# Performance work log

Measured on AMD Instinct MI355X. Metric: run time of the kernel, lower is better.

The kernel has to match this reference:

```python
import jax, jax.numpy as jnp
import numpy as np

D_MODEL = 1024
D_FF = 2048
N_EXPERTS = 8
Z_LOSS_COEF = 0.001


def setup_inputs() -> dict:
    key = jax.random.key(0)
    kx, kr, k1, k3, k2 = jax.random.split(key, 5)
    s_in = 1.0 / np.sqrt(D_MODEL)
    s_ff = 1.0 / np.sqrt(D_FF)
    return {
        "x": jax.random.normal(kx, (4, 2048, D_MODEL), dtype=jnp.float32),
        # router: nn.Linear(d_model, num_experts, bias=False) -> weight [E, D]
        "Wr": jax.random.normal(kr, (N_EXPERTS, D_MODEL), dtype=jnp.float32) * s_in,
        # stacked expert weights, torch Linear layout [out, in]
        "W1": jax.random.normal(k1, (N_EXPERTS, D_FF, D_MODEL), dtype=jnp.float32) * s_in,
        "W3": jax.random.normal(k3, (N_EXPERTS, D_FF, D_MODEL), dtype=jnp.float32) * s_in,
        "W2": jax.random.normal(k2, (N_EXPERTS, D_MODEL, D_FF), dtype=jnp.float32) * s_ff,
    }


def reference(x, Wr, W1, W3, W2):
    B, S, D = x.shape
    E = Wr.shape[0]
    xf = x.reshape(B * S, D)          # [T, D]
    T = xf.shape[0]

    # --- router ---
    logits = xf @ Wr.T                # [T, E]
    probs = jax.nn.softmax(logits, axis=-1)
    top2_p, top2_i = jax.lax.top_k(probs, 2)          # [T, 2]
    top2_p = top2_p / (jnp.sum(top2_p, axis=-1, keepdims=True) + 1e-9)

    # dense gate matrix: zero for unselected experts (same math as index_add combine)
    gates = jnp.zeros((T, E), jnp.float32).at[jnp.arange(T)[:, None], top2_i].add(top2_p)

    # --- experts (SwiGLU), computed per-expert over all tokens, masked by gates ---
    h1 = jax.nn.silu(jnp.einsum('td,efd->etf', xf, W1))   # [E, T, F]
    h3 = jnp.einsum('td,efd->etf', xf, W3)                 # [E, T, F]
    y = jnp.einsum('etf,edf->etd', h1 * h3, W2)            # [E, T, D]
    out = jnp.einsum('etd,te->td', y.astype(jnp.float32), gates)
    out = out.astype(x.dtype).reshape(B, S, D)

    # --- losses ---
    z = jax.nn.logsumexp(logits.astype(jnp.float32), axis=-1)
    router_loss = Z_LOSS_COEF * jnp.mean(z * z)

    importance = jnp.sum(probs.astype(jnp.float32), axis=0) / T   # [E]
    top1 = top2_i[:, 0]
    load = jnp.zeros((E,), jnp.float32).at[top1].add(1.0) / T
    aux_loss = jnp.sum(importance * load) * E

    return out, router_loss, aux_loss
```

## Files before the change

### kernel.cpp

```cpp
#include <hip/hip_runtime.h>
#include <stdint.h>

#define NT 8192
#define DM 1024
#define DF 2048
#define RT_BLOCKS 256

typedef __attribute__((ext_vector_type(8))) short short8;
typedef __attribute__((ext_vector_type(4))) float f32x4;
typedef unsigned short us;

__device__ __forceinline__ us f2bf(float f) {
  uint32_t x = __float_as_uint(f);
  return (us)((x + 0x7fffu + ((x >> 16) & 1u)) >> 16);
}

__device__ __forceinline__ void gload16(const void* g, void* l) {
  __builtin_amdgcn_global_load_lds(
      (const __attribute__((address_space(1))) uint32_t*)g,
      (__attribute__((address_space(3))) uint32_t*)l, 16, 0, 0);
}

__global__ void k_cvtw(const float4* __restrict__ w1, const float4* __restrict__ w3,
                       const float4* __restrict__ w2,
                       ushort4* __restrict__ w13, ushort4* __restrict__ w2bf) {
  int s = blockIdx.y;
  const float4* src = (s == 0) ? w1 : (s == 1) ? w3 : w2;
  int n4 = 8 * DF * DM / 4;
  int i = blockIdx.x * blockDim.x + threadIdx.x;
  int st = gridDim.x * blockDim.x;
  for (; i < n4; i += st) {
    float4 v = src[i];
    ushort4 o;
    o.x = f2bf(v.x); o.y = f2bf(v.y); o.z = f2bf(v.z); o.w = f2bf(v.w);
    if (s == 2) {
      w2bf[i] = o;
    } else {
      int e = i >> 19;
      int rem = i & ((1 << 19) - 1);
      int f = rem >> 8;
      int k4 = rem & 255;
      w13[((size_t)e << 20) + (size_t)(2 * f + s) * 256 + k4] = o;
    }
  }
}

__global__ void k_router(const float* __restrict__ x, const float* __restrict__ wr,
                         int* cntb, int* cnt1, float* imp, float* z2,
                         int* epack, float2* gts, us* __restrict__ xbf) {
  int lane = threadIdx.x & 63;
  int wid = threadIdx.x >> 6;
  const float4* w4 = (const float4*)wr;

  float imp_acc[8] = {0.f, 0.f, 0.f, 0.f, 0.f, 0.f, 0.f, 0.f};
  float z2_acc = 0.f;
  int cb_acc[8] = {0, 0, 0, 0, 0, 0, 0, 0};
  int c1_acc[8] = {0, 0, 0, 0, 0, 0, 0, 0};

  for (int t = blockIdx.x * 4 + wid; t < NT; t += RT_BLOCKS * 4) {
    const float4* x4 = (const float4*)(x + (size_t)t * DM);
    ushort4* xb4 = (ushort4*)(xbf + (size_t)t * DM);
    float4 xv[4];
    #pragma unroll
    for (int j = 0; j < 4; ++j) {
      xv[j] = x4[lane + 64 * j];
      ushort4 o;
      o.x = f2bf(xv[j].x); o.y = f2bf(xv[j].y); o.z = f2bf(xv[j].z); o.w = f2bf(xv[j].w);
      xb4[lane + 64 * j] = o;
    }
    float p[8];
    #pragma unroll
    for (int e = 0; e < 8; ++e) p[e] = 0.f;
    #pragma unroll
    for (int j = 0; j < 4; ++j) {
      #pragma unroll
      for (int e = 0; e < 8; ++e) {
        float4 wv = w4[e * 256 + lane + 64 * j];
        p[e] += xv[j].x * wv.x + xv[j].y * wv.y + xv[j].z * wv.z + xv[j].w * wv.w;
      }
    }
    #pragma unroll
    for (int off = 32; off > 0; off >>= 1) {
      #pragma unroll
      for (int e = 0; e < 8; ++e) p[e] += __shfl_down(p[e], off);
    }
    if (lane == 0) {
      float m = p[0];
      #pragma unroll
      for (int e = 1; e < 8; ++e) m = fmaxf(m, p[e]);
      float pr[8], s = 0.f;
      #pragma unroll
      for (int e = 0; e < 8; ++e) { pr[e] = expf(p[e] - m); s += pr[e]; }
      float inv = 1.f / s;
      #pragma unroll
      for (int e = 0; e < 8; ++e) pr[e] *= inv;
      float z = m + logf(s);
      int e0 = 0; float b0 = p[0];
      #pragma unroll
      for (int e = 1; e < 8; ++e) { if (p[e] > b0) { b0 = p[e]; e0 = e; } }
      int e1 = -1; float b1 = -1e30f;
      #pragma unroll
      for (int e = 0; e < 8; ++e) { if (e != e0 && p[e] > b1) { b1 = p[e]; e1 = e; } }
      float p0 = 0.f, p1 = 0.f;
      #pragma unroll
      for (int e = 0; e < 8; ++e) {
        p0 = (e == e0) ? pr[e] : p0;
        p1 = (e == e1) ? pr[e] : p1;
      }
      float gs = p0 + p1 + 1e-9f;
      epack[t] = e0 | (e1 << 16);
      gts[t] = make_float2(p0 / gs, p1 / gs);
      z2_acc += z * z;
      #pragma unroll
      for (int e = 0; e < 8; ++e) {
        imp_acc[e] += pr[e];
        cb_acc[e] += (e == e0) + (e == e1);
        c1_acc[e] += (e == e0);
      }
    }
  }

  __shared__ float simp[4][8];
  __shared__ float sz2[4];
  __shared__ int scb[4][8];
  __shared__ int sc1[4][8];
  if (lane == 0) {
    #pragma unroll
    for (int e = 0; e < 8; ++e) { simp[wid][e] = imp_acc[e]; scb[wid][e] = cb_acc[e]; sc1[wid][e] = c1_acc[e]; }
    sz2[wid] = z2_acc;
  }
  __syncthreads();
  int tid = threadIdx.x;
  if (tid < 8) {
    float s = simp[0][tid] + simp[1][tid] + simp[2][tid] + simp[3][tid];
    int b = scb[0][tid] + scb[1][tid] + scb[2][tid] + scb[3][tid];
    int o = sc1[0][tid] + sc1[1][tid] + sc1[2][tid] + sc1[3][tid];
    atomicAdd(&imp[tid], s);
    atomicAdd(&cntb[tid], b);
    atomicAdd(&cnt1[tid], o);
  } else if (tid == 8) {
    atomicAdd(z2, sz2[0] + sz2[1] + sz2[2] + sz2[3]);
  }
}

__global__ void k_finalize(const int* cntb, const int* cnt1, const float* imp,
                           const float* z2, int* offs, float* otail) {
  if (threadIdx.x == 0 && blockIdx.x == 0) {
    int o = 0;
    for (int e = 0; e < 8; ++e) { offs[e] = o; o += cntb[e]; }
    otail[0] = 1e-3f * z2[0] / (float)NT;
    float aux = 0.f;
    for (int e = 0; e < 8; ++e)
      aux += (imp[e] / (float)NT) * ((float)cnt1[e] / (float)NT);
    otail[1] = aux * 8.f;
  }
}

__global__ void k_scatter(const int* __restrict__ epack, const float2* __restrict__ gts,
                          const int* __restrict__ offs,
                          int* __restrict__ btok, int* __restrict__ pos) {
  int e = blockIdx.x;
  int lane = threadIdx.x;
  int base = offs[e];
  int run = 0;
  for (int j0 = 0; j0 < 2 * NT; j0 += 64) {
    int j = j0 + lane;
    int t = j >> 1;
    int ep = epack[t];
    int sel = (j & 1) ? (ep >> 16) : (ep & 0xffff);
    bool f = (sel == e);
    unsigned long long m = __ballot(f);
    int rank = __popcll(m & ((1ull << lane) - 1ull));
    if (f) {
      int slot = base + run + rank;
      btok[slot] = t;
      pos[j] = slot;
    }
    run += __popcll(m);
  }
}


__global__ __launch_bounds__(512) void k_ffn1(
    const us* __restrict__ xb, const us* __restrict__ w13,
    const int* __restrict__ offs, const int* __restrict__ cnts,
    const int* __restrict__ btok, us* __restrict__ hg) {
  int e = blockIdx.z;
  int cnt = cnts[e];
  int m0 = blockIdx.y * 256;
  if (m0 >= cnt) return;
  int n0 = blockIdx.x * 256;
  int off = offs[e];
  __shared__ __align__(16) short As[2][8192];
  __shared__ __align__(16) short Bs[2][8192];
  __shared__ int tok[256];
  int tid = threadIdx.x, lane = tid & 63, wid = tid >> 6;
  if (tid < 256) {
    int r = m0 + tid; if (r > cnt - 1) r = cnt - 1;
    tok[tid] = btok[off + r];
  }
  __syncthreads();

  int posun = (lane & 7) ^ ((lane >> 3) & 7);
  int rbase = wid * 16 + ((lane >> 3) << 1) + (posun >> 2);
  int gcol = (posun & 3) * 8;
  const us* w13e = w13 + ((size_t)e << 22);
  const us* aP0 = xb + (size_t)tok[rbase] * DM + gcol;
  const us* aP1 = xb + (size_t)tok[rbase + 128] * DM + gcol;
  const us* bP0 = w13e + (size_t)(n0 + rbase) * DM + gcol;
  const us* bP1 = w13e + (size_t)(n0 + rbase + 128) * DM + gcol;
  int dst0 = wid * 512, dst1 = 4096 + wid * 512;

  int wm = wid >> 2, wn = wid & 3;
  int fr = lane & 15, glog = lane >> 4;
  int pos = (((fr & 1) << 2) | glog) ^ ((fr >> 1) & 7);
  int aoff = (wm * 64 + (fr >> 1)) * 64 + pos * 8;
  int boff = (wn * 32 + (fr >> 1)) * 64 + pos * 8;
  f32x4 acc[8][4] = {};

  const int NK = DM / 64;
  for (int kt = 0; kt < NK; ++kt) {
    int k0 = kt * 64;
    #pragma unroll
    for (int h = 0; h < 2; ++h) {
      int ko = k0 + h * 32;
      gload16(aP0 + ko, &As[h][dst0]);
      gload16(aP1 + ko, &As[h][dst1]);
      gload16(bP0 + ko, &Bs[h][dst0]);
      gload16(bP1 + ko, &Bs[h][dst1]);
    }
    __syncthreads();
    #pragma unroll
    for (int kk = 0; kk < 2; ++kk) {
      short8 a[8], b[4];
      #pragma unroll
      for (int mi = 0; mi < 8; ++mi)
        a[mi] = *(const short8*)&As[kk][aoff + mi * 512];
      #pragma unroll
      for (int ni = 0; ni < 4; ++ni)
        b[ni] = *(const short8*)&Bs[kk][boff + ni * 512];
      #pragma unroll
      for (int mi = 0; mi < 8; ++mi) {
        #pragma unroll
        for (int ni = 0; ni < 4; ++ni)
          acc[mi][ni] = __builtin_amdgcn_mfma_f32_16x16x32_bf16(a[mi], b[ni], acc[mi][ni], 0, 0, 0);
      }
    }
    __syncthreads();
  }

  int c = lane & 15, r4 = (lane >> 4) * 4;
  bool evenc = ((c & 1) == 0);
  #pragma unroll
  for (int mi = 0; mi < 8; ++mi) {
    #pragma unroll
    for (int rg = 0; rg < 4; ++rg) {
      int gr = m0 + wm * 128 + mi * 16 + r4 + rg;
      #pragma unroll
      for (int ni = 0; ni < 4; ++ni) {
        float a1v = acc[mi][ni][rg];
        float a3v = __shfl_xor(a1v, 1);
        if (evenc && gr < cnt) {
          int f = (n0 + wn * 64 + ni * 16 + c) >> 1;
          float h = (a1v / (1.f + __expf(-a1v))) * a3v;
          hg[(size_t)(off + gr) * DF + f] = f2bf(h);
        }
      }
    }
  }
}

__global__ __launch_bounds__(512) void k_ffn2(
    const us* __restrict__ hg, const us* __restrict__ w2b,
    const int* __restrict__ offs, const int* __restrict__ cnts,
    float* __restrict__ ys) {
  int e = blockIdx.z;
  int cnt = cnts[e];
  int m0 = blockIdx.y * 256;
  if (m0 >= cnt) return;
  int n0 = blockIdx.x * 256;
  int off = offs[e];
  __shared__ __align__(16) short As[2][8192];
  __shared__ __align__(16) short Bs[2][8192];
  int tid = threadIdx.x, lane = tid & 63, wid = tid >> 6;

  int posun = (lane & 7) ^ ((lane >> 3) & 7);
  int rbase = wid * 16 + ((lane >> 3) << 1) + (posun >> 2);
  int gcol = (posun & 3) * 8;
  int ar0 = m0 + rbase;       if (ar0 > cnt - 1) ar0 = cnt - 1;
  int ar1 = m0 + rbase + 128; if (ar1 > cnt - 1) ar1 = cnt - 1;
  const us* w2e = w2b + ((size_t)e << 21);
  const us* aP0 = hg + (size_t)(off + ar0) * DF + gcol;
  const us* aP1 = hg + (size_t)(off + ar1) * DF + gcol;
  const us* bP0 = w2e + (size_t)(n0 + rbase) * DF + gcol;
  const us* bP1 = w2e + (size_t)(n0 + rbase + 128) * DF + gcol;
  int dst0 = wid * 512, dst1 = 4096 + wid * 512;

  int wm = wid >> 2, wn = wid & 3;
  int fr = lane & 15, glog = lane >> 4;
  int pos = (((fr & 1) << 2) | glog) ^ ((fr >> 1) & 7);
  int aoff = (wm * 64 + (fr >> 1)) * 64 + pos * 8;
  int boff = (wn * 32 + (fr >> 1)) * 64 + pos * 8;
  f32x4 acc[8][4] = {};

  const int NK = DF / 64;
  for (int kt = 0; kt < NK; ++kt) {
    int k0 = kt * 64;
    #pragma unroll
    for (int h = 0; h < 2; ++h) {
      int ko = k0 + h * 32;
      gload16(aP0 + ko, &As[h][dst0]);
      gload16(aP1 + ko, &As[h][dst1]);
      gload16(bP0 + ko, &Bs[h][dst0]);
      gload16(bP1 + ko, &Bs[h][dst1]);
    }
    __syncthreads();
    #pragma unroll
    for (int kk = 0; kk < 2; ++kk) {
      short8 a[8], b[4];
      #pragma unroll
      for (int mi = 0; mi < 8; ++mi)
        a[mi] = *(const short8*)&As[kk][aoff + mi * 512];
      #pragma unroll
      for (int ni = 0; ni < 4; ++ni)
        b[ni] = *(const short8*)&Bs[kk][boff + ni * 512];
      #pragma unroll
      for (int mi = 0; mi < 8; ++mi) {
        #pragma unroll
        for (int ni = 0; ni < 4; ++ni)
          acc[mi][ni] = __builtin_amdgcn_mfma_f32_16x16x32_bf16(a[mi], b[ni], acc[mi][ni], 0, 0, 0);
      }
    }
    __syncthreads();
  }

  int c = lane & 15, r4 = (lane >> 4) * 4;
  #pragma unroll
  for (int mi = 0; mi < 8; ++mi) {
    #pragma unroll
    for (int rg = 0; rg < 4; ++rg) {
      int gr = m0 + wm * 128 + mi * 16 + r4 + rg;
      if (gr < cnt) {
        float* yrow = ys + (size_t)(off + gr) * DM + n0;
        #pragma unroll
        for (int ni = 0; ni < 4; ++ni)
          yrow[wn * 64 + ni * 16 + c] = acc[mi][ni][rg];
      }
    }
  }
}

__global__ void k_gather(const float* __restrict__ ys, const int* __restrict__ pos,
                         const float2* __restrict__ gts, float* __restrict__ out) {
  int idx = blockIdx.x * blockDim.x + threadIdx.x;
  int t = idx >> 8;
  int d4 = idx & 255;
  float2 g = gts[t];
  const float4* y0 = (const float4*)(ys + (size_t)pos[2 * t] * DM) + d4;
  const float4* y1 = (const float4*)(ys + (size_t)pos[2 * t + 1] * DM) + d4;
  float4 a = *y0, b = *y1, o;
  o.x = g.x * a.x + g.y * b.x;
  o.y = g.x * a.y + g.y * b.y;
  o.z = g.x * a.z + g.y * b.z;
  o.w = g.x * a.w + g.y * b.w;
  ((float4*)out)[idx] = o;
}


extern "C" void kernel_launch(void* const* d_in, const int* in_sizes, int n_in,
                              void* d_out, int out_size, void* d_ws, size_t ws_size,
                              hipStream_t stream) {
  const float* x  = (const float*)d_in[0];
  const float* wr = (const float*)d_in[1];
  const float* w1 = (const float*)d_in[2];
  const float* w3 = (const float*)d_in[3];
  const float* w2 = (const float*)d_in[4];
  float* out = (float*)d_out;

  uint8_t* ws = (uint8_t*)d_ws;
  int*    cntb   = (int*)(ws + 0);
  int*    cnt1   = (int*)(ws + 32);
  int*    offs   = (int*)(ws + 96);
  float*  imp    = (float*)(ws + 128);
  float*  z2     = (float*)(ws + 160);
  int*    epack  = (int*)(ws + 4096);
  float2* gts    = (float2*)(ws + 36864);
  int*    btok   = (int*)(ws + 102400);
  int*    pos    = (int*)(ws + 167936);
  us*     xbf    = (us*)(ws + 233472);
  us*     w13    = (us*)(ws + 17010688);
  us*     w2bf   = (us*)(ws + 84119552);
  us*     hg     = (us*)(ws + 117673984);
  float*  ysb    = (float*)(ws + 17010688);

  hipMemsetAsync(ws, 0, 4096, stream);

  k_cvtw<<<dim3(2048, 3), 256, 0, stream>>>(
      (const float4*)w1, (const float4*)w3, (const float4*)w2,
      (ushort4*)w13, (ushort4*)w2bf);

  k_router<<<RT_BLOCKS, 256, 0, stream>>>(x, wr, cntb, cnt1, imp, z2, epack, gts, xbf);
  k_finalize<<<1, 64, 0, stream>>>(cntb, cnt1, imp, z2, offs, out + (size_t)NT * DM);
  k_scatter<<<8, 64, 0, stream>>>(epack, gts, offs, btok, pos);

  k_ffn1<<<dim3(16, 64, 8), 512, 0, stream>>>(xbf, w13, offs, cntb, btok, hg);
  k_ffn2<<<dim3(4, 64, 8), 512, 0, stream>>>(hg, w2bf, offs, cntb, ysb);
  k_gather<<<NT * DM / 4 / 256, 256, 0, stream>>>(ysb, pos, gts, out);
}
```

Measured before the change: 617.5 us.

## Shrink FFN GEMM tiles to 128x128, store expert outputs as bf16, interleave W1/W3 by 16

```diff
diff --git a/kernel.cpp b/kernel.cpp
--- a/kernel.cpp
+++ b/kernel.cpp
@@ -14,6 +14,9 @@
   uint32_t x = __float_as_uint(f);
   return (us)((x + 0x7fffu + ((x >> 16) & 1u)) >> 16);
 }
+__device__ __forceinline__ float bf2f(us v) {
+  return __uint_as_float(((uint32_t)v) << 16);
+}
 
 __device__ __forceinline__ void gload16(const void* g, void* l) {
   __builtin_amdgcn_global_load_lds(
@@ -23,24 +26,28 @@
 
 __global__ void k_cvtw(const float4* __restrict__ w1, const float4* __restrict__ w3,
                        const float4* __restrict__ w2,
-                       ushort4* __restrict__ w13, ushort4* __restrict__ w2bf) {
+                       short8* __restrict__ w13, short8* __restrict__ w2bf) {
   int s = blockIdx.y;
   const float4* src = (s == 0) ? w1 : (s == 1) ? w3 : w2;
-  int n4 = 8 * DF * DM / 4;
+  int n8 = 8 * DF * DM / 8;
   int i = blockIdx.x * blockDim.x + threadIdx.x;
   int st = gridDim.x * blockDim.x;
-  for (; i < n4; i += st) {
-    float4 v = src[i];
-    ushort4 o;
-    o.x = f2bf(v.x); o.y = f2bf(v.y); o.z = f2bf(v.z); o.w = f2bf(v.w);
+  for (; i < n8; i += st) {
+    float4 va = src[2 * i], vb = src[2 * i + 1];
+    short8 o;
+    o[0] = (short)f2bf(va.x); o[1] = (short)f2bf(va.y);
+    o[2] = (short)f2bf(va.z); o[3] = (short)f2bf(va.w);
+    o[4] = (short)f2bf(vb.x); o[5] = (short)f2bf(vb.y);
+    o[6] = (short)f2bf(vb.z); o[7] = (short)f2bf(vb.w);
     if (s == 2) {
       w2bf[i] = o;
     } else {
-      int e = i >> 19;
-      int rem = i & ((1 << 19) - 1);
-      int f = rem >> 8;
-      int k4 = rem & 255;
-      w13[((size_t)e << 20) + (size_t)(2 * f + s) * 256 + k4] = o;
+      int e = i >> 18;
+      int rem = i & ((1 << 18) - 1);
+      int f = rem >> 7;
+      int k8 = rem & 127;
+      int n = 32 * (f >> 4) + 16 * s + (f & 15);
+      w13[((size_t)e << 19) + (size_t)n * 128 + k8] = o;
     }
   }
 }
@@ -88,13 +95,13 @@
       float m = p[0];
       #pragma unroll
       for (int e = 1; e < 8; ++e) m = fmaxf(m, p[e]);
-      float pr[8], s = 0.f;
-      #pragma unroll
-      for (int e = 0; e < 8; ++e) { pr[e] = expf(p[e] - m); s += pr[e]; }
-      float inv = 1.f / s;
+      float pr[8], sum = 0.f;
+      #pragma unroll
+      for (int e = 0; e < 8; ++e) { pr[e] = expf(p[e] - m); sum += pr[e]; }
+      float inv = 1.f / sum;
       #pragma unroll
       for (int e = 0; e < 8; ++e) pr[e] *= inv;
-      float z = m + logf(s);
+      float z = m + logf(sum);
       int e0 = 0; float b0 = p[0];
       #pragma unroll
       for (int e = 1; e < 8; ++e) { if (p[e] > b0) { b0 = p[e]; e0 = e; } }
@@ -132,10 +139,10 @@
   __syncthreads();
   int tid = threadIdx.x;
   if (tid < 8) {
-    float s = simp[0][tid] + simp[1][tid] + simp[2][tid] + simp[3][tid];
+    float ss = simp[0][tid] + simp[1][tid] + simp[2][tid] + simp[3][tid];
     int b = scb[0][tid] + scb[1][tid] + scb[2][tid] + scb[3][tid];
     int o = sc1[0][tid] + sc1[1][tid] + sc1[2][tid] + sc1[3][tid];
-    atomicAdd(&imp[tid], s);
+    atomicAdd(&imp[tid], ss);
     atomicAdd(&cntb[tid], b);
     atomicAdd(&cnt1[tid], o);
   } else if (tid == 8) {
@@ -181,42 +188,43 @@
 }
 
 
-__global__ __launch_bounds__(512) void k_ffn1(
+__global__ __launch_bounds__(256) void k_ffn1(
     const us* __restrict__ xb, const us* __restrict__ w13,
     const int* __restrict__ offs, const int* __restrict__ cnts,
     const int* __restrict__ btok, us* __restrict__ hg) {
   int e = blockIdx.z;
   int cnt = cnts[e];
-  int m0 = blockIdx.y * 256;
+  int m0 = blockIdx.y * 128;
   if (m0 >= cnt) return;
-  int n0 = blockIdx.x * 256;
+  int n0 = blockIdx.x * 128;
   int off = offs[e];
-  __shared__ __align__(16) short As[2][8192];
-  __shared__ __align__(16) short Bs[2][8192];
-  __shared__ int tok[256];
+  __shared__ __align__(16) short As[2][4096];
+  __shared__ __align__(16) short Bs[2][4096];
+  __shared__ int tok[128];
   int tid = threadIdx.x, lane = tid & 63, wid = tid >> 6;
-  if (tid < 256) {
+  if (tid < 128) {
     int r = m0 + tid; if (r > cnt - 1) r = cnt - 1;
     tok[tid] = btok[off + r];
   }
   __syncthreads();
 
-  int posun = (lane & 7) ^ ((lane >> 3) & 7);
-  int rbase = wid * 16 + ((lane >> 3) << 1) + (posun >> 2);
-  int gcol = (posun & 3) * 8;
+  int prow = tid >> 3;
+  int pu = (tid & 7) ^ (prow & 7);
+  int row0 = prow * 2 + (pu >> 2);
+  int gc = (pu & 3) * 8;
   const us* w13e = w13 + ((size_t)e << 22);
-  const us* aP0 = xb + (size_t)tok[rbase] * DM + gcol;
-  const us* aP1 = xb + (size_t)tok[rbase + 128] * DM + gcol;
-  const us* bP0 = w13e + (size_t)(n0 + rbase) * DM + gcol;
-  const us* bP1 = w13e + (size_t)(n0 + rbase + 128) * DM + gcol;
-  int dst0 = wid * 512, dst1 = 4096 + wid * 512;
-
-  int wm = wid >> 2, wn = wid & 3;
+  const us* a0 = xb + (size_t)tok[row0] * DM + gc;
+  const us* a1 = xb + (size_t)tok[row0 + 64] * DM + gc;
+  const us* b0 = w13e + (size_t)(n0 + row0) * DM + gc;
+  const us* b1 = w13e + (size_t)(n0 + row0 + 64) * DM + gc;
+  int dsl = tid * 8;
+
+  int wm = wid >> 1, wn = wid & 1;
   int fr = lane & 15, glog = lane >> 4;
   int pos = (((fr & 1) << 2) | glog) ^ ((fr >> 1) & 7);
-  int aoff = (wm * 64 + (fr >> 1)) * 64 + pos * 8;
+  int aoff = (wm * 32 + (fr >> 1)) * 64 + pos * 8;
   int boff = (wn * 32 + (fr >> 1)) * 64 + pos * 8;
-  f32x4 acc[8][4] = {};
+  f32x4 acc[4][4] = {};
 
   const int NK = DM / 64;
   for (int kt = 0; kt < NK; ++kt) {
@@ -224,23 +232,21 @@
     #pragma unroll
     for (int h = 0; h < 2; ++h) {
       int ko = k0 + h * 32;
-      gload16(aP0 + ko, &As[h][dst0]);
-      gload16(aP1 + ko, &As[h][dst1]);
-      gload16(bP0 + ko, &Bs[h][dst0]);
-      gload16(bP1 + ko, &Bs[h][dst1]);
+      gload16(a0 + ko, &As[h][dsl]);
+      gload16(a1 + ko, &As[h][dsl + 2048]);
+      gload16(b0 + ko, &Bs[h][dsl]);
+      gload16(b1 + ko, &Bs[h][dsl + 2048]);
     }
     __syncthreads();
     #pragma unroll
-    for (int kk = 0; kk < 2; ++kk) {
-      short8 a[8], b[4];
-      #pragma unroll
-      for (int mi = 0; mi < 8; ++mi)
-        a[mi] = *(const short8*)&As[kk][aoff + mi * 512];
-      #pragma unroll
-      for (int ni = 0; ni < 4; ++ni)
-        b[ni] = *(const short8*)&Bs[kk][boff + ni * 512];
-      #pragma unroll
-      for (int mi = 0; mi < 8; ++mi) {
+    for (int h = 0; h < 2; ++h) {
+      short8 a[4], b[4];
+      #pragma unroll
+      for (int mi = 0; mi < 4; ++mi) a[mi] = *(const short8*)&As[h][aoff + mi * 512];
+      #pragma unroll
+      for (int ni = 0; ni < 4; ++ni) b[ni] = *(const short8*)&Bs[h][boff + ni * 512];
+      #pragma unroll
+      for (int mi = 0; mi < 4; ++mi) {
         #pragma unroll
         for (int ni = 0; ni < 4; ++ni)
           acc[mi][ni] = __builtin_amdgcn_mfma_f32_16x16x32_bf16(a[mi], b[ni], acc[mi][ni], 0, 0, 0);
@@ -250,58 +256,59 @@
   }
 
   int c = lane & 15, r4 = (lane >> 4) * 4;
-  bool evenc = ((c & 1) == 0);
+  int fb = (n0 + wn * 64) >> 1;
   #pragma unroll
-  for (int mi = 0; mi < 8; ++mi) {
+  for (int mi = 0; mi < 4; ++mi) {
     #pragma unroll
     for (int rg = 0; rg < 4; ++rg) {
-      int gr = m0 + wm * 128 + mi * 16 + r4 + rg;
-      #pragma unroll
-      for (int ni = 0; ni < 4; ++ni) {
-        float a1v = acc[mi][ni][rg];
-        float a3v = __shfl_xor(a1v, 1);
-        if (evenc && gr < cnt) {
-          int f = (n0 + wn * 64 + ni * 16 + c) >> 1;
+      int gr = m0 + wm * 64 + mi * 16 + r4 + rg;
+      if (gr < cnt) {
+        us* hrow = hg + (size_t)(off + gr) * DF;
+        #pragma unroll
+        for (int j = 0; j < 2; ++j) {
+          float a1v = acc[mi][2 * j][rg];
+          float a3v = acc[mi][2 * j + 1][rg];
           float h = (a1v / (1.f + __expf(-a1v))) * a3v;
-          hg[(size_t)(off + gr) * DF + f] = f2bf(h);
+          hrow[fb + j * 16 + c] = f2bf(h);
         }
       }
     }
   }
 }
 
-__global__ __launch_bounds__(512) void k_ffn2(
+__global__ __launch_bounds__(256) void k_ffn2(
     const us* __restrict__ hg, const us* __restrict__ w2b,
     const int* __restrict__ offs, const int* __restrict__ cnts,
-    float* __restrict__ ys) {
+    us* __restrict__ ys) {
   int e = blockIdx.z;
   int cnt = cnts[e];
-  int m0 = blockIdx.y * 256;
+  int m0 = blockIdx.y * 128;
   if (m0 >= cnt) return;
-  int n0 = blockIdx.x * 256;
+  int n0 = blockIdx.x * 128;
   int off = offs[e];
-  __shared__ __align__(16) short As[2][8192];
-  __shared__ __align__(16) short Bs[2][8192];
+  __shared__ __align__(16) short As[2][4096];
+  __shared__ __align__(16) short Bs[2][4096];
   int tid = threadIdx.x, lane = tid & 63, wid = tid >> 6;
 
-  int posun = (lane & 7) ^ ((lane >> 3) & 7);
-  int rbase = wid * 16 + ((lane >> 3) << 1) + (posun >> 2);
-  int gcol = (posun & 3) * 8;
-  int ar0 = m0 + rbase;       if (ar0 > cnt - 1) ar0 = cnt - 1;
-  int ar1 = m0 + rbase + 128; if (ar1 > cnt - 1) ar1 = cnt - 1;
+  int prow = tid >> 3;
+  int pu = (tid & 7) ^ (prow & 7);
+  int row0 = prow * 2 + (pu >> 2);
+  int gc = (pu & 3) * 8;
+  int ar0 = m0 + row0;      if (ar0 > cnt - 1) ar0 = cnt - 1;
+  int ar1 = m0 + row0 + 64; if (ar1 > cnt - 1) ar1 = cnt - 1;
   const us* w2e = w2b + ((size_t)e << 21);
-  const us* aP0 = hg + (size_t)(off + ar0) * DF + gcol;
-  const us* aP1 = hg + (size_t)(off + ar1) * DF + gcol;
-  const us* bP0 = w2e + (size_t)(n0 + rbase) * DF + gcol;
-  const us* bP1 = w2e + (size_t)(n0 + rbase + 128) * DF + gcol;
-  int dst0 = wid * 512, dst1 = 4096 + wid * 512;
-
-  int wm = wid >> 2, wn = wid & 3;
+  const us* a0 = hg + (size_t)(off + ar0) * DF + gc;
+  const us* a1 = hg + (size_t)(off + ar1) * DF + gc;
+  const us* b0 = w2e + (size_t)(n0 + row0) * DF + gc;
+  const us* b1 = w2e + (size_t)(n0 + row0 + 64) * DF + gc;
+  int dsl = tid * 8;
+
+  int wm = wid >> 1, wn = wid & 1;
   int fr = lane & 15, glog = lane >> 4;
   int pos = (((fr & 1) << 2) | glog) ^ ((fr >> 1) & 7);
-  int aoff = (wm * 64 + (fr >> 1)) * 64 + pos * 8;
+  int aoff = (wm * 32 + (fr >> 1)) * 64 + pos * 8;
   int boff = (wn * 32 + (fr >> 1)) * 64 + pos * 8;
-  f32x4 acc[8][4] = {};
+  f32x4 acc[4][4] = {};
 
   const int NK = DF / 64;
   for (int kt = 0; kt < NK; ++kt) {
@@ -309,23 +316,21 @@
     #pragma unroll
     for (int h = 0; h < 2; ++h) {
       int ko = k0 + h * 32;
-      gload16(aP0 + ko, &As[h][dst0]);
-      gload16(aP1 + ko, &As[h][dst1]);
-      gload16(bP0 + ko, &Bs[h][dst0]);
-      gload16(bP1 + ko, &Bs[h][dst1]);
+      gload16(a0 + ko, &As[h][dsl]);
+      gload16(a1 + ko, &As[h][dsl + 2048]);
+      gload16(b0 + ko, &Bs[h][dsl]);
+      gload16(b1 + ko, &Bs[h][dsl + 2048]);
     }
     __syncthreads();
     #pragma unroll
-    for (int kk = 0; kk < 2; ++kk) {
-      short8 a[8], b[4];
-      #pragma unroll
-      for (int mi = 0; mi < 8; ++mi)
-        a[mi] = *(const short8*)&As[kk][aoff + mi * 512];
-      #pragma unroll
-      for (int ni = 0; ni < 4; ++ni)
-        b[ni] = *(const short8*)&Bs[kk][boff + ni * 512];
-      #pragma unroll
-      for (int mi = 0; mi < 8; ++mi) {
+    for (int h = 0; h < 2; ++h) {
+      short8 a[4], b[4];
+      #pragma unroll
+      for (int mi = 0; mi < 4; ++mi) a[mi] = *(const short8*)&As[h][aoff + mi * 512];
+      #pragma unroll
+      for (int ni = 0; ni < 4; ++ni) b[ni] = *(const short8*)&Bs[h][boff + ni * 512];
+      #pragma unroll
+      for (int mi = 0; mi < 4; ++mi) {
         #pragma unroll
         for (int ni = 0; ni < 4; ++ni)
           acc[mi][ni] = __builtin_amdgcn_mfma_f32_16x16x32_bf16(a[mi], b[ni], acc[mi][ni], 0, 0, 0);
@@ -336,33 +341,33 @@
 
   int c = lane & 15, r4 = (lane >> 4) * 4;
   #pragma unroll
-  for (int mi = 0; mi < 8; ++mi) {
+  for (int mi = 0; mi < 4; ++mi) {
     #pragma unroll
     for (int rg = 0; rg < 4; ++rg) {
-      int gr = m0 + wm * 128 + mi * 16 + r4 + rg;
+      int gr = m0 + wm * 64 + mi * 16 + r4 + rg;
       if (gr < cnt) {
-        float* yrow = ys + (size_t)(off + gr) * DM + n0;
+        us* yrow = ys + (size_t)(off + gr) * DM + n0;
         #pragma unroll
         for (int ni = 0; ni < 4; ++ni)
-          yrow[wn * 64 + ni * 16 + c] = acc[mi][ni][rg];
-      }
-    }
-  }
-}
-
-__global__ void k_gather(const float* __restrict__ ys, const int* __restrict__ pos,
+          yrow[wn * 64 + ni * 16 + c] = f2bf(acc[mi][ni][rg]);
+      }
+    }
+  }
+}
+
+__global__ void k_gather(const us* __restrict__ ys, const int* __restrict__ pos,
                          const float2* __restrict__ gts, float* __restrict__ out) {
   int idx = blockIdx.x * blockDim.x + threadIdx.x;
   int t = idx >> 8;
   int d4 = idx & 255;
   float2 g = gts[t];
-  const float4* y0 = (const float4*)(ys + (size_t)pos[2 * t] * DM) + d4;
-  const float4* y1 = (const float4*)(ys + (size_t)pos[2 * t + 1] * DM) + d4;
-  float4 a = *y0, b = *y1, o;
-  o.x = g.x * a.x + g.y * b.x;
-  o.y = g.x * a.y + g.y * b.y;
-  o.z = g.x * a.z + g.y * b.z;
-  o.w = g.x * a.w + g.y * b.w;
+  ushort4 a = ((const ushort4*)(ys + (size_t)pos[2 * t] * DM))[d4];
+  ushort4 b = ((const ushort4*)(ys + (size_t)pos[2 * t + 1] * DM))[d4];
+  float4 o;
+  o.x = g.x * bf2f(a.x) + g.y * bf2f(b.x);
+  o.y = g.x * bf2f(a.y) + g.y * bf2f(b.y);
+  o.z = g.x * bf2f(a.z) + g.y * bf2f(b.z);
+  o.w = g.x * bf2f(a.w) + g.y * bf2f(b.w);
   ((float4*)out)[idx] = o;
 }
 
@@ -391,19 +396,19 @@
   us*     w13    = (us*)(ws + 17010688);
   us*     w2bf   = (us*)(ws + 84119552);
   us*     hg     = (us*)(ws + 117673984);
-  float*  ysb    = (float*)(ws + 17010688);
+  us*     ysb    = (us*)(ws + 17010688);
 
   hipMemsetAsync(ws, 0, 4096, stream);
 
+  k_router<<<RT_BLOCKS, 256, 0, stream>>>(x, wr, cntb, cnt1, imp, z2, epack, gts, xbf);
   k_cvtw<<<dim3(2048, 3), 256, 0, stream>>>(
       (const float4*)w1, (const float4*)w3, (const float4*)w2,
-      (ushort4*)w13, (ushort4*)w2bf);
-
-  k_router<<<RT_BLOCKS, 256, 0, stream>>>(x, wr, cntb, cnt1, imp, z2, epack, gts, xbf);
+      (short8*)w13, (short8*)w2bf);
+
   k_finalize<<<1, 64, 0, stream>>>(cntb, cnt1, imp, z2, offs, out + (size_t)NT * DM);
   k_scatter<<<8, 64, 0, stream>>>(epack, gts, offs, btok, pos);
 
-  k_ffn1<<<dim3(16, 64, 8), 512, 0, stream>>>(xbf, w13, offs, cntb, btok, hg);
-  k_ffn2<<<dim3(4, 64, 8), 512, 0, stream>>>(hg, w2bf, offs, cntb, ysb);
+  k_ffn1<<<dim3(32, 128, 8), 256, 0, stream>>>(xbf, w13, offs, cntb, btok, hg);
+  k_ffn2<<<dim3(8, 128, 8), 256, 0, stream>>>(hg, w2bf, offs, cntb, ysb);
   k_gather<<<NT * DM / 4 / 256, 256, 0, stream>>>(ysb, pos, gts, out);
 }
```

Result: faster. 503.7 us (-18.4%).
